# Kernel tuning notes

Hardware: AMD Instinct MI355X
Metric: run time of the kernel (lower is better)

Reference implementation:

```python
import jax, jax.numpy as jnp
import numpy as np

LAM = 0.5   # dec_init_lambda
NEG = -1e8  # attention mask fill


def gru_cell(x, h, W_ih, W_hh, b_ih, b_hh):
    # torch.nn.GRUCell math
    gi = x @ W_ih.T + b_ih
    gh = h @ W_hh.T + b_hh
    ir, iz, inn = jnp.split(gi, 3, axis=-1)
    hr, hz, hn = jnp.split(gh, 3, axis=-1)
    r = jax.nn.sigmoid(ir + hr)
    z = jax.nn.sigmoid(iz + hz)
    n = jnp.tanh(inn + r * hn)
    return (1.0 - z) * n + z * h


def setup_inputs() -> dict:
    key = jax.random.key(0)
    S, B, C, H, E, V, TY = 64, 64, 512, 512, 512, 32000, 49
    ks = jax.random.split(key, 16)
    sc = lambda d: 1.0 / float(np.sqrt(d))
    inp = {}
    inp['ctx'] = jax.random.normal(ks[0], (S, B, C), jnp.float32)
    inp['ctx_mask'] = jnp.ones((S, B), jnp.float32)
    inp['txt_ctx'] = jax.random.normal(ks[1], (B, C), jnp.float32)
    inp['y'] = jax.random.randint(ks[2], (TY, B), 0, V)
    emb = jax.random.normal(ks[3], (V, E), jnp.float32) * 0.01
    inp['emb_table'] = emb.at[0].set(0.0)  # padding_idx=0
    inp['W_ctx2ctx'] = jax.random.normal(ks[4], (C, C), jnp.float32) * sc(C)
    inp['W_hid2ctx'] = jax.random.normal(ks[5], (C, H), jnp.float32) * sc(H)
    inp['w_mlp'] = jax.random.normal(ks[6], (C,), jnp.float32) * sc(C)
    inp['W_ctx2hid'] = jax.random.normal(ks[7], (H, C), jnp.float32) * sc(C)
    inp['W_dec_init'] = jax.random.normal(ks[8], (H, C), jnp.float32) * sc(C)
    inp['W_ih0'] = jax.random.normal(ks[9], (3 * H, E), jnp.float32) * sc(E)
    inp['W_hh0'] = jax.random.normal(ks[10], (3 * H, H), jnp.float32) * sc(H)
    inp['b_ih0'] = jnp.zeros((3 * H,), jnp.float32)
    inp['b_hh0'] = jnp.zeros((3 * H,), jnp.float32)
    inp['W_ih1'] = jax.random.normal(ks[11], (3 * H, H), jnp.float32) * sc(H)
    inp['W_hh1'] = jax.random.normal(ks[12], (3 * H, H), jnp.float32) * sc(H)
    inp['b_ih1'] = jnp.zeros((3 * H,), jnp.float32)
    inp['b_hh1'] = jnp.zeros((3 * H,), jnp.float32)
    inp['W_hid2out'] = jax.random.normal(ks[13], (E, H), jnp.float32) * sc(H)
    inp['b_hid2out'] = jnp.zeros((E,), jnp.float32)  # bias_zero=True
    inp['W_out2prob'] = jax.random.normal(ks[14], (V, E), jnp.float32) * sc(E)
    inp['b_out2prob'] = jnp.zeros((V,), jnp.float32)
    return inp


def reference(ctx, ctx_mask, txt_ctx, y, emb_table,
              W_ctx2ctx, W_hid2ctx, w_mlp, W_ctx2hid, W_dec_init,
              W_ih0, W_hh0, b_ih0, b_hh0,
              W_ih1, W_hh1, b_ih1, b_hh1,
              W_hid2out, b_hid2out, W_out2prob, b_out2prob):
    # f_init: mix mean visual ctx with sentence ctx, project to h0
    mean_ctx = ctx.sum(0) / ctx_mask.sum(0)[:, None]          # (B, C)
    mixed = LAM * mean_ctx + (1.0 - LAM) * txt_ctx            # (B, C)
    h0 = jnp.tanh(mixed @ W_dec_init.T)                       # (B, H)

    # precompute ctx projection of MLP attention (ctx2ctx), shared across steps
    ctx_proj = jnp.einsum('sbc,mc->sbm', ctx, W_ctx2ctx)      # (S, B, C)

    x_seq = emb_table[y[:-1]]                                 # (T, B, E) teacher-forced inputs
    tgt = y[1:]                                               # (T, B) targets

    def step(h, xs):
        x, t = xs
        h1 = gru_cell(x, h, W_ih0, W_hh0, b_ih0, b_hh0)       # (B, H)
        q = h1 @ W_hid2ctx.T                                  # (B, C)
        scores = jnp.einsum('sbm,m->sb', jnp.tanh(ctx_proj + q[None]), w_mlp)
        scores = jnp.where(ctx_mask > 0, scores, NEG)
        alpha = jax.nn.softmax(scores, axis=0)                # (S, B) over source
        z_t = jnp.einsum('sb,sbc->bc', alpha, ctx) @ W_ctx2hid.T  # (B, H)
        h2 = gru_cell(z_t, h1, W_ih1, W_hh1, b_ih1, b_hh1)    # (B, H)
        logit = jnp.tanh(h2 @ W_hid2out.T + b_hid2out)        # (B, E)
        log_p = jax.nn.log_softmax(logit @ W_out2prob.T + b_out2prob, axis=-1)
        lp = jnp.take_along_axis(log_p, t[:, None], axis=1)[:, 0]
        loss_t = -jnp.where(t != 0, lp, 0.0).sum()            # NLLLoss(sum, ignore_index=0)
        return h2, loss_t

    _, losses = jax.lax.scan(step, h0, (x_seq, tgt))
    return losses.sum()
```

## Files before the change

kernel.cpp:

```cpp
#include <hip/hip_runtime.h>
#include <stdint.h>


using bf16x8 = __attribute__((ext_vector_type(8))) short;
using f32x4  = __attribute__((ext_vector_type(4))) float;
using s16x4  = __attribute__((ext_vector_type(4))) short;
typedef unsigned long long u64;
typedef unsigned int u32;

#define DI __device__ __forceinline__

DI short f2bf(float x){
  union { float f; uint32_t u; } v; v.f = x;
  uint32_t r = (v.u + 0x7FFFu + ((v.u >> 16) & 1u)) >> 16;
  return (short)r;
}
DI float bf2f(short s){
  union { uint32_t u; float f; } v; v.u = ((uint32_t)(unsigned short)s) << 16; return v.f;
}
DI float sigm(float x){ return __fdividef(1.f, 1.f + __expf(-x)); }
DI float ftanh(float x){ return 1.f - __fdividef(2.f, __expf(2.f*x) + 1.f); }
DI float wsum(float v){
  #pragma unroll
  for (int m = 32; m > 0; m >>= 1) v += __shfl_xor(v, m, 64);
  return v;
}
DI f32x4 mfma16(bf16x8 a, bf16x8 b, f32x4 c){
  return __builtin_amdgcn_mfma_f32_16x16x32_bf16(a, b, c, 0, 0, 0);
}

DI u32  ald32(const u32* p){ return __hip_atomic_load(p, __ATOMIC_RELAXED, __HIP_MEMORY_SCOPE_AGENT); }
DI void ast32(u32* p, u32 v){ __hip_atomic_store(p, v, __ATOMIC_RELAXED, __HIP_MEMORY_SCOPE_AGENT); }
DI u64  ald64(const u64* p){ return __hip_atomic_load(p, __ATOMIC_RELAXED, __HIP_MEMORY_SCOPE_AGENT); }
DI void ast64(u64* p, u64 v){ __hip_atomic_store(p, v, __ATOMIC_RELAXED, __HIP_MEMORY_SCOPE_AGENT); }
DI float aldf(const float* p){ return __hip_atomic_load(p, __ATOMIC_RELAXED, __HIP_MEMORY_SCOPE_AGENT); }
DI void astf(float* p, float v){ __hip_atomic_store(p, v, __ATOMIC_RELAXED, __HIP_MEMORY_SCOPE_AGENT); }

DI bf16x8 ldb(const short* __restrict__ W, int n0, int k0, int lane){
  return *(const bf16x8*)(W + (size_t)(n0 + (lane & 15)) * 512 + k0 + ((lane >> 4) << 3));
}

#define SLOT 64

DI void sig(u32* arr, int slot, u32 tok){
  if (threadIdx.x == 0){
    __builtin_amdgcn_s_waitcnt(0);
    ast32(arr + slot * SLOT, tok);
  }
}
DI void waitslots(const u32* arr, int base, int cnt, u32 tok){
  if (threadIdx.x < 64){
    for (;;){
      u32 v = (threadIdx.x < cnt) ? ald32(arr + (base + threadIdx.x) * SLOT) : tok;
      if (__all((int)(v - tok) >= 0)) break;
      __builtin_amdgcn_s_sleep(1);
    }
  }
  __syncthreads();
}


struct CvtJobs { const float* src[8]; short* dst[8]; int cum4[9]; };

__global__ __launch_bounds__(256) void k_cvt_multi(CvtJobs jb, int total4){
  int i = blockIdx.x * 256 + threadIdx.x;
  if (i >= total4) return;
  int j = 0;
  #pragma unroll
  for (int k = 0; k < 8; ++k) if (i >= jb.cum4[k + 1]) j = k + 1;
  int off = i - jb.cum4[j];
  float4 v = ((const float4*)jb.src[j])[off];
  s16x4 o; o[0] = f2bf(v.x); o[1] = f2bf(v.y); o[2] = f2bf(v.z); o[3] = f2bf(v.w);
  ((s16x4*)jb.dst[j])[off] = o;
}

__global__ __launch_bounds__(256) void k_tc(const float* __restrict__ W, short* __restrict__ WT){
  int i = blockIdx.x * 256 + threadIdx.x;
  int c = i >> 9, h = i & 511;
  WT[i] = f2bf(W[h * 512 + c]);
}

__global__ __launch_bounds__(256) void k_zero(float* __restrict__ p, int n){
  int i = blockIdx.x * 256 + threadIdx.x;
  if (i < n) p[i] = 0.f;
}

__global__ __launch_bounds__(256) void k_meanmix(const float* __restrict__ ctx, const float* __restrict__ mask,
                                                 const float* __restrict__ txt, float* __restrict__ mixed){
  int i = blockIdx.x * 256 + threadIdx.x;
  int b = i >> 9, c = i & 511;
  float s = 0.f;
  for (int t = 0; t < 64; ++t) s += ctx[(size_t)(t * 64 + b) * 512 + c];
  float dn = 0.f;
  for (int t = 0; t < 64; ++t) dn += mask[t * 64 + b];
  mixed[i] = 0.5f * (s / dn) + 0.5f * txt[i];
}

__global__ __launch_bounds__(256) void k_pack_h0(const float* __restrict__ h0, u32* __restrict__ hbf){
  int i = blockIdx.x * 256 + threadIdx.x;
  u32 lo = (u32)(unsigned short)f2bf(h0[2 * i]);
  u32 hi = (u32)(unsigned short)f2bf(h0[2 * i + 1]);
  hbf[i] = lo | (hi << 16);
}


DI bf16x8 load_a32(const float* __restrict__ A, int ld, int m0, int k0, int lane){
  const float* p = A + (size_t)(m0 + (lane & 15)) * ld + k0 + ((lane >> 4) << 3);
  bf16x8 f;
  #pragma unroll
  for (int j = 0; j < 8; ++j) f[j] = f2bf(p[j]);
  return f;
}

__global__ __launch_bounds__(256) void k_gemm_bt(const float* __restrict__ A, const short* __restrict__ W,
                                                 float* __restrict__ C, int N, int act){
  int wg = blockIdx.x * 4 + (threadIdx.x >> 6);
  int lane = threadIdx.x & 63;
  int ntiles = N >> 4;
  int mt = wg / ntiles, nt = wg - mt * ntiles;
  int m0 = mt << 4, n0 = nt << 4;
  f32x4 acc = {0.f, 0.f, 0.f, 0.f};
  for (int k = 0; k < 512; k += 32)
    acc = mfma16(load_a32(A, 512, m0, k, lane), ldb(W, n0, k, lane), acc);
  int col = n0 + (lane & 15);
  int r0 = m0 + ((lane >> 4) << 2);
  #pragma unroll
  for (int r = 0; r < 4; ++r){
    float v = acc[r];
    if (act) v = ftanh(v);
    C[(size_t)(r0 + r) * N + col] = v;
  }
}

__global__ __launch_bounds__(256) void k_gemm_bt_obf(const float* __restrict__ A, const short* __restrict__ W,
                                                     short* __restrict__ C, int N){
  int wg = blockIdx.x * 4 + (threadIdx.x >> 6);
  int lane = threadIdx.x & 63;
  int ntiles = N >> 4;
  int mt = wg / ntiles, nt = wg - mt * ntiles;
  int m0 = mt << 4, n0 = nt << 4;
  f32x4 acc = {0.f, 0.f, 0.f, 0.f};
  for (int k = 0; k < 512; k += 32)
    acc = mfma16(load_a32(A, 512, m0, k, lane), ldb(W, n0, k, lane), acc);
  int col = n0 + (lane & 15);
  int r0 = m0 + ((lane >> 4) << 2);
  #pragma unroll
  for (int r = 0; r < 4; ++r)
    C[(size_t)(r0 + r) * N + col] = f2bf(acc[r]);
}

__global__ __launch_bounds__(256) void k_gi0(const int* __restrict__ y, const float* __restrict__ emb,
                                             const short* __restrict__ W, const float* __restrict__ bias,
                                             float* __restrict__ C){
  int wg = blockIdx.x * 4 + (threadIdx.x >> 6);
  int lane = threadIdx.x & 63;
  int mt = wg / 96, nt = wg - mt * 96;
  int m0 = mt << 4, n0 = nt << 4;
  int yr = y[m0 + (lane & 15)];
  const float* arow = emb + (size_t)yr * 512;
  f32x4 acc = {0.f, 0.f, 0.f, 0.f};
  for (int k = 0; k < 512; k += 32){
    const float* p = arow + k + ((lane >> 4) << 3);
    bf16x8 a;
    #pragma unroll
    for (int j = 0; j < 8; ++j) a[j] = f2bf(p[j]);
    acc = mfma16(a, ldb(W, n0, k, lane), acc);
  }
  int col = n0 + (lane & 15);
  int r0 = m0 + ((lane >> 4) << 2);
  #pragma unroll
  for (int r = 0; r < 4; ++r)
    C[(size_t)(r0 + r) * 1536 + col] = acc[r] + bias[col];
}


struct RB {
  const float* gi0;
  const short* Whh0; const float* bhh0;
  const short* Whid2ctx;
  const short* Whh1; const float* bhh1;
  const short* Wcomb; const float* bih1;
  const short* ctx_proj;
  const float* ctx;
  const float* mask;
  const float* wmlp;
  unsigned short* h_bf;
  unsigned short* h1_bf;
  unsigned short* catt_bf;
  float* qpart;
  float* h2;
  u32* barA; u32* barC; u32* barD;
};

__global__ __launch_bounds__(256, 1) void k_recur(RB a){
  __shared__ char smem[16 * 520 * 2 + 16 * 64 * 4];
  unsigned short* sH = (unsigned short*)smem;
  float* sOut = (float*)(smem + 16 * 520 * 2);
  float* pl   = (float*)smem;
  __shared__ float qs[512];
  __shared__ float al[64];
  const int wg = blockIdx.x, tid = threadIdx.x;
  const int wv = tid >> 6, lane = tid & 63;

  auto burst16 = [&](const unsigned short* src, int row0){
    #pragma unroll
    for (int i = 0; i < 8; ++i){
      int idx = tid + i * 256;
      int r = idx >> 7, c4 = idx & 127;
      u64 v = ald64((const u64*)(src + (size_t)(row0 + r) * 512) + c4);
      *(u64*)(sH + r * 520 + c4 * 4) = v;
    }
    __syncthreads();
  };
  auto afrag = [&](int k0) -> bf16x8 {
    return *(const bf16x8*)(sH + (lane & 15) * 520 + k0 + ((lane >> 4) << 3));
  };
  auto packstore = [&](unsigned short* dst, int mrow0, int jbase){
    int r = tid >> 4, ch = tid & 15;
    float4 v = *(const float4*)&sOut[r * 64 + ch * 4];
    u64 pk = (u64)(unsigned short)f2bf(v.x)
           | ((u64)(unsigned short)f2bf(v.y) << 16)
           | ((u64)(unsigned short)f2bf(v.z) << 32)
           | ((u64)(unsigned short)f2bf(v.w) << 48);
    ast64((u64*)(dst + (size_t)(mrow0 + r) * 512 + jbase + ch * 4), pk);
  };
  auto attention = [&](int b, float maskv, const float (&w8)[8]){
    float q0 = 0.f, q1 = 0.f;
    #pragma unroll
    for (int cgi = 0; cgi < 8; ++cgi){
      u64 v = ald64((const u64*)(a.qpart + (size_t)(cgi * 64 + b) * 512) + tid);
      union { u64 u; float f[2]; } cv; cv.u = v;
      q0 += cv.f[0]; q1 += cv.f[1];
    }
    qs[2 * tid] = q0; qs[2 * tid + 1] = q1;
    __syncthreads();
    float q8[8];
    #pragma unroll
    for (int j = 0; j < 8; ++j) q8[j] = qs[lane * 8 + j];
    for (int i = 0; i < 16; ++i){
      int s = (wv << 4) + i;
      bf16x8 c8 = *(const bf16x8*)(a.ctx_proj + (size_t)((s << 6) + b) * 512 + lane * 8);
      float p = 0.f;
      #pragma unroll
      for (int j = 0; j < 8; ++j)
        p += ftanh(bf2f(c8[j]) + q8[j]) * w8[j];
      pl[s * 65 + lane] = p;
    }
    __syncthreads();
    if (tid < 64){
      const float* row = pl + tid * 65;
      float v0 = 0.f, v1 = 0.f, v2 = 0.f, v3 = 0.f;
      #pragma unroll
      for (int j = 0; j < 64; j += 4){
        v0 += row[j]; v1 += row[j + 1]; v2 += row[j + 2]; v3 += row[j + 3];
      }
      float v = (v0 + v1) + (v2 + v3);
      v = (maskv > 0.f) ? v : -100000000.0f;
      float mx = v;
      #pragma unroll
      for (int m = 32; m > 0; m >>= 1) mx = fmaxf(mx, __shfl_xor(mx, m, 64));
      float e = __expf(v - mx);
      float se = e;
      #pragma unroll
      for (int m = 32; m > 0; m >>= 1) se += __shfl_xor(se, m, 64);
      al[tid] = e / se;
    }
    __syncthreads();
    float s0 = 0.f, s1 = 0.f;
    int c0 = tid * 2;
    for (int s = 0; s < 64; ++s){
      float2 cv = *(const float2*)(a.ctx + (size_t)((s << 6) + b) * 512 + c0);
      s0 += al[s] * cv.x; s1 += al[s] * cv.y;
    }
    u32 pk = (u32)(unsigned short)f2bf(s0) | ((u32)(unsigned short)f2bf(s1) << 16);
    ast32((u32*)a.catt_bf + (size_t)b * 256 + tid, pk);
  };

  if (wg < 32){
    const int rg = wg >> 3, cg = wg & 7;
    const int mrow0 = rg << 4, jbase = cg << 6;
    const int j0 = jbase + (wv << 4);
    const int col = j0 + (lane & 15), lcol = col - jbase;
    const int lr0 = (lane >> 4) << 2;
    const int batt = wg;
    const int abase = (batt >> 4) << 3;
    const float bh0r = a.bhh0[col], bh0z = a.bhh0[512 + col], bh0n = a.bhh0[1024 + col];
    float w8[8];
    #pragma unroll
    for (int j = 0; j < 8; ++j) w8[j] = a.wmlp[lane * 8 + j];
    const float maskv = (tid < 64) ? a.mask[(tid << 6) + batt] : 0.f;
    float g0[4], g1[4], g2[4];
    {
      const float* gi = a.gi0;
      #pragma unroll
      for (int r = 0; r < 4; ++r){
        const float* gib = gi + (size_t)(mrow0 + lr0 + r) * 1536;
        g0[r] = gib[col]; g1[r] = gib[512 + col]; g2[r] = gib[1024 + col];
      }
    }
    #pragma unroll 1
    for (int t = 0; t < 48; ++t){
      const u32 tok = t + 1;
      waitslots(a.barD, rg << 3, 8, (u32)t);
      burst16(a.h_bf, mrow0);
      f32x4 aR = {0,0,0,0}, aZ = {0,0,0,0}, aN = {0,0,0,0};
      for (int k0 = 0; k0 < 512; k0 += 32){
        bf16x8 af = afrag(k0);
        aR = mfma16(af, ldb(a.Whh0, j0,        k0, lane), aR);
        aZ = mfma16(af, ldb(a.Whh0, 512 + j0,  k0, lane), aZ);
        aN = mfma16(af, ldb(a.Whh0, 1024 + j0, k0, lane), aN);
      }
      #pragma unroll
      for (int r = 0; r < 4; ++r){
        int lr = lr0 + r;
        float rr = sigm(g0[r] + aR[r] + bh0r);
        float zz = sigm(g1[r] + aZ[r] + bh0z);
        float nn = ftanh(g2[r] + rr * (aN[r] + bh0n));
        float hp = bf2f((short)sH[lr * 520 + col]);
        sOut[lr * 64 + lcol] = (1.f - zz) * nn + zz * hp;
      }
      __syncthreads();
      packstore(a.h1_bf, mrow0, jbase);
      bf16x8 qa0, qa1;
      #pragma unroll
      for (int j = 0; j < 8; ++j){
        qa0[j] = f2bf(sOut[(lane & 15) * 64 +      ((lane >> 4) << 3) + j]);
        qa1[j] = f2bf(sOut[(lane & 15) * 64 + 32 + ((lane >> 4) << 3) + j]);
      }
      #pragma unroll
      for (int nt = 0; nt < 8; ++nt){
        int n0 = (wv << 7) + (nt << 4);
        f32x4 qacc = {0,0,0,0};
        qacc = mfma16(qa0, ldb(a.Whid2ctx, n0, jbase,      lane), qacc);
        qacc = mfma16(qa1, ldb(a.Whid2ctx, n0, jbase + 32, lane), qacc);
        int qcol = n0 + (lane & 15);
        #pragma unroll
        for (int r = 0; r < 4; ++r)
          astf(a.qpart + (size_t)(cg * 64 + mrow0 + lr0 + r) * 512 + qcol, qacc[r]);
      }
      __syncthreads();
      sig(a.barA, wg, tok);
      waitslots(a.barA, abase, 8, tok);
      attention(batt, maskv, w8);
      __syncthreads();
      sig(a.barC, batt, tok);
      if (t < 47){
        const float* gi = a.gi0 + (size_t)(t + 1) * 98304;
        #pragma unroll
        for (int r = 0; r < 4; ++r){
          const float* gib = gi + (size_t)(mrow0 + lr0 + r) * 1536;
          g0[r] = gib[col]; g1[r] = gib[512 + col]; g2[r] = gib[1024 + col];
        }
      }
    }
  } else if (wg < 64){
    const int g = wg - 32;
    const int rg = g >> 3, cg = g & 7;
    const int mrow0 = rg << 4, jbase = cg << 6;
    const int j0 = jbase + (wv << 4);
    const int col = j0 + (lane & 15), lcol = col - jbase;
    const int lr0 = (lane >> 4) << 2;
    const float bcR = a.bih1[col]        + a.bhh1[col];
    const float bcZ = a.bih1[512 + col]  + a.bhh1[512 + col];
    const float biN = a.bih1[1024 + col];
    const float bhN = a.bhh1[1024 + col];
    #pragma unroll 1
    for (int t = 0; t < 48; ++t){
      const u32 tok = t + 1;
      waitslots(a.barA, rg << 3, 8, tok);
      burst16(a.h1_bf, mrow0);
      f32x4 hR = {0,0,0,0}, hZ = {0,0,0,0}, hN = {0,0,0,0};
      for (int k0 = 0; k0 < 512; k0 += 32){
        bf16x8 af = afrag(k0);
        hR = mfma16(af, ldb(a.Whh1, j0,        k0, lane), hR);
        hZ = mfma16(af, ldb(a.Whh1, 512 + j0,  k0, lane), hZ);
        hN = mfma16(af, ldb(a.Whh1, 1024 + j0, k0, lane), hN);
      }
      float hp4[4];
      #pragma unroll
      for (int r = 0; r < 4; ++r) hp4[r] = bf2f((short)sH[(lr0 + r) * 520 + col]);
      waitslots(a.barC, mrow0, 16, tok);
      burst16(a.catt_bf, mrow0);
      f32x4 iR = {0,0,0,0}, iZ = {0,0,0,0}, iN = {0,0,0,0};
      for (int k0 = 0; k0 < 512; k0 += 32){
        bf16x8 af = afrag(k0);
        iR = mfma16(af, ldb(a.Wcomb, j0,        k0, lane), iR);
        iZ = mfma16(af, ldb(a.Wcomb, 512 + j0,  k0, lane), iZ);
        iN = mfma16(af, ldb(a.Wcomb, 1024 + j0, k0, lane), iN);
      }
      float* h2t = a.h2 + (size_t)t * 32768;
      #pragma unroll
      for (int r = 0; r < 4; ++r){
        int lr = lr0 + r, b = mrow0 + lr;
        float rr = sigm(iR[r] + hR[r] + bcR);
        float zz = sigm(iZ[r] + hZ[r] + bcZ);
        float nn = ftanh(iN[r] + biN + rr * (hN[r] + bhN));
        float hv = (1.f - zz) * nn + zz * hp4[r];
        h2t[(size_t)b * 512 + col] = hv;
        sOut[lr * 64 + lcol] = hv;
      }
      __syncthreads();
      packstore(a.h_bf, mrow0, jbase);
      __syncthreads();
      sig(a.barD, g, tok);
    }
  } else {
    const int b = wg - 32;
    const int abase = (b >> 4) << 3;
    float w8[8];
    #pragma unroll
    for (int j = 0; j < 8; ++j) w8[j] = a.wmlp[lane * 8 + j];
    const float maskv = (tid < 64) ? a.mask[(tid << 6) + b] : 0.f;
    #pragma unroll 1
    for (int t = 0; t < 48; ++t){
      const u32 tok = t + 1;
      waitslots(a.barA, abase, 8, tok);
      attention(b, maskv, w8);
      __syncthreads();
      sig(a.barC, b, tok);
    }
  }
}


__global__ __launch_bounds__(256) void k_logit(const float* __restrict__ A, const short* __restrict__ W,
                                               const float* __restrict__ bias, short* __restrict__ tlb,
                                               float* __restrict__ tlf){
  int wg = blockIdx.x * 4 + (threadIdx.x >> 6);
  int lane = threadIdx.x & 63;
  int mt = wg >> 5, nt = wg & 31;
  int m0 = mt << 4, n0 = nt << 4;
  f32x4 acc = {0.f, 0.f, 0.f, 0.f};
  for (int k = 0; k < 512; k += 32)
    acc = mfma16(load_a32(A, 512, m0, k, lane), ldb(W, n0, k, lane), acc);
  int col = n0 + (lane & 15);
  int r0 = m0 + ((lane >> 4) << 2);
  #pragma unroll
  for (int r = 0; r < 4; ++r){
    float v = ftanh(acc[r] + bias[col]);
    size_t o = (size_t)(r0 + r) * 512 + col;
    tlf[o] = v; tlb[o] = f2bf(v);
  }
}

__global__ __launch_bounds__(256) void k_sumexp(const short* __restrict__ A, const short* __restrict__ B,
                                                const float* __restrict__ bias, float* __restrict__ sumexp){
  __shared__ short lA[128 * 40];
  __shared__ short lB[128 * 40];
  int bid = blockIdx.x;
  int swz = (bid & 7) * 750 + (bid >> 3);
  int bm = swz % 24, bn = swz / 24;
  int m0 = bm * 128, n0 = bn * 128;
  int tid = threadIdx.x, w = tid >> 6, lane = tid & 63;
  int mq = (w >> 1) * 64, nq = (w & 1) * 64;
  f32x4 acc[4][4];
  #pragma unroll
  for (int i = 0; i < 4; ++i)
    #pragma unroll
    for (int j = 0; j < 4; ++j) acc[i][j] = (f32x4){0.f, 0.f, 0.f, 0.f};

  for (int k0 = 0; k0 < 512; k0 += 32){
    __syncthreads();
    #pragma unroll
    for (int i = 0; i < 2; ++i){
      int idx = tid * 8 + i * 2048;
      int row = idx >> 5, colh = idx & 31;
      *(bf16x8*)&lA[row * 40 + colh] = *(const bf16x8*)(A + (size_t)(m0 + row) * 512 + k0 + colh);
      *(bf16x8*)&lB[row * 40 + colh] = *(const bf16x8*)(B + (size_t)(n0 + row) * 512 + k0 + colh);
    }
    __syncthreads();
    bf16x8 af[4], bfr[4];
    #pragma unroll
    for (int x = 0; x < 4; ++x){
      af[x]  = *(const bf16x8*)&lA[(mq + x * 16 + (lane & 15)) * 40 + ((lane >> 4) << 3)];
      bfr[x] = *(const bf16x8*)&lB[(nq + x * 16 + (lane & 15)) * 40 + ((lane >> 4) << 3)];
    }
    #pragma unroll
    for (int mi = 0; mi < 4; ++mi)
      #pragma unroll
      for (int ni = 0; ni < 4; ++ni)
        acc[mi][ni] = mfma16(af[mi], bfr[ni], acc[mi][ni]);
  }

  #pragma unroll
  for (int mi = 0; mi < 4; ++mi){
    #pragma unroll
    for (int r = 0; r < 4; ++r){
      float e = 0.f;
      #pragma unroll
      for (int ni = 0; ni < 4; ++ni){
        int col = n0 + nq + ni * 16 + (lane & 15);
        e += __expf(acc[mi][ni][r] + bias[col]);
      }
      e += __shfl_xor(e, 1, 64); e += __shfl_xor(e, 2, 64);
      e += __shfl_xor(e, 4, 64); e += __shfl_xor(e, 8, 64);
      if ((lane & 15) == 0){
        int row = m0 + mq + mi * 16 + ((lane >> 4) << 2) + r;
        atomicAdd(&sumexp[row], e);
      }
    }
  }
}

__global__ __launch_bounds__(256) void k_loss(const float* __restrict__ tlf, const float* __restrict__ Wop,
                                              const float* __restrict__ bop, const int* __restrict__ y,
                                              const float* __restrict__ sumexp, float* __restrict__ loss){
  int step = blockIdx.x;
  int w = threadIdx.x >> 6, lane = threadIdx.x & 63;
  __shared__ float accw[4];
  float part = 0.f;
  for (int b = w; b < 64; b += 4){
    int row = step * 64 + b;
    int t = y[(step + 1) * 64 + b];
    if (t != 0){
      const float* a = tlf + (size_t)row * 512 + lane * 8;
      const float* wr = Wop + (size_t)t * 512 + lane * 8;
      float d = 0.f;
      #pragma unroll
      for (int j = 0; j < 8; ++j) d += a[j] * wr[j];
      d = wsum(d);
      if (lane == 0) part += d + bop[t] - __logf(sumexp[row]);
    }
  }
  if (lane == 0) accw[w] = part;
  __syncthreads();
  if (threadIdx.x == 0) atomicAdd(loss, -(accw[0] + accw[1] + accw[2] + accw[3]));
}

__global__ void k_final(const float* __restrict__ loss, float* __restrict__ out){
  if (threadIdx.x == 0 && blockIdx.x == 0) out[0] = loss[0];
}


extern "C" void kernel_launch(void* const* d_in, const int* in_sizes, int n_in,
                              void* d_out, int out_size, void* d_ws, size_t ws_size,
                              hipStream_t stream) {
  const float* ctx       = (const float*)d_in[0];
  const float* ctx_mask  = (const float*)d_in[1];
  const float* txt_ctx   = (const float*)d_in[2];
  const int*   y         = (const int*)d_in[3];
  const float* emb       = (const float*)d_in[4];
  const float* W_ctx2ctx = (const float*)d_in[5];
  const float* W_hid2ctx = (const float*)d_in[6];
  const float* w_mlp     = (const float*)d_in[7];
  const float* W_ctx2hid = (const float*)d_in[8];
  const float* W_dec_init= (const float*)d_in[9];
  const float* W_ih0     = (const float*)d_in[10];
  const float* W_hh0     = (const float*)d_in[11];
  const float* b_ih0     = (const float*)d_in[12];
  const float* b_hh0     = (const float*)d_in[13];
  const float* W_ih1     = (const float*)d_in[14];
  const float* W_hh1     = (const float*)d_in[15];
  const float* b_ih1     = (const float*)d_in[16];
  const float* b_hh1     = (const float*)d_in[17];
  const float* W_hid2out = (const float*)d_in[18];
  const float* b_hid2out = (const float*)d_in[19];
  const float* W_out2prob= (const float*)d_in[20];
  const float* b_out2prob= (const float*)d_in[21];
  float* out = (float*)d_out;

  char* p = (char*)d_ws;
  auto alloc = [&](size_t n){ char* r = p; p += (n + 255) & ~(size_t)255; return r; };
  short* Wb_hh0     = (short*)alloc((size_t)1536 * 512 * 2);
  short* Wb_hid2ctx = (short*)alloc((size_t)512 * 512 * 2);
  short* Wb_hh1     = (short*)alloc((size_t)1536 * 512 * 2);
  short* Wb_hid2out = (short*)alloc((size_t)512 * 512 * 2);
  short* Wb_dec     = (short*)alloc((size_t)512 * 512 * 2);
  short* Wb_c2c     = (short*)alloc((size_t)512 * 512 * 2);
  short* Wb_ih0     = (short*)alloc((size_t)1536 * 512 * 2);
  short* Wb_o2p     = (short*)alloc((size_t)32000 * 512 * 2);
  short* WctT       = (short*)alloc((size_t)512 * 512 * 2);
  short* Wb_comb    = (short*)alloc((size_t)1536 * 512 * 2);
  short* ctx_projbf = (short*)alloc((size_t)4096 * 512 * 2);
  float* gi0_all    = (float*)alloc((size_t)3072 * 1536 * 4);
  float* mixed      = (float*)alloc((size_t)64 * 512 * 4);
  float* h0buf      = (float*)alloc((size_t)64 * 512 * 4);
  unsigned short* h_bf    = (unsigned short*)alloc((size_t)64 * 512 * 2);
  unsigned short* h1_bf   = (unsigned short*)alloc((size_t)64 * 512 * 2);
  unsigned short* catt_bf = (unsigned short*)alloc((size_t)64 * 512 * 2);
  float* qpart      = (float*)alloc((size_t)8 * 64 * 512 * 4);
  float* h2_all     = (float*)alloc((size_t)3072 * 512 * 4);
  short* tl_bf      = (short*)alloc((size_t)3072 * 512 * 2);
  float* tl_f       = (float*)alloc((size_t)3072 * 512 * 4);
  int nbar = 3 * 64 * SLOT;
  float* zreg       = (float*)alloc((size_t)(3073 + nbar) * 4);
  float* sumexp     = zreg;
  float* lossbuf    = zreg + 3072;
  u32* barA         = (u32*)(zreg + 3073);
  u32* barC         = barA + 64 * SLOT;
  u32* barD         = barC + 64 * SLOT;

  dim3 blk(256);
  CvtJobs jb;
  const float* srcs[8] = {W_hh0, W_hid2ctx, W_hh1, W_hid2out, W_dec_init, W_ctx2ctx, W_ih0, W_out2prob};
  short* dsts[8] = {Wb_hh0, Wb_hid2ctx, Wb_hh1, Wb_hid2out, Wb_dec, Wb_c2c, Wb_ih0, Wb_o2p};
  int sizes4[8] = {1536*512/4, 512*512/4, 1536*512/4, 512*512/4, 512*512/4, 512*512/4, 1536*512/4, 32000*512/4};
  int cum = 0;
  for (int i = 0; i < 8; ++i){ jb.src[i] = srcs[i]; jb.dst[i] = dsts[i]; jb.cum4[i] = cum; cum += sizes4[i]; }
  jb.cum4[8] = cum;
  k_cvt_multi<<<dim3((cum + 255) / 256), blk, 0, stream>>>(jb, cum);
  k_tc<<<dim3(1024), blk, 0, stream>>>(W_ctx2hid, WctT);
  k_gemm_bt_obf<<<dim3(768), blk, 0, stream>>>(W_ih1, WctT, Wb_comb, 512);
  k_meanmix<<<dim3(128), blk, 0, stream>>>(ctx, ctx_mask, txt_ctx, mixed);
  k_gemm_bt<<<dim3(32), blk, 0, stream>>>(mixed, Wb_dec, h0buf, 512, 1);
  k_pack_h0<<<dim3(64), blk, 0, stream>>>(h0buf, (u32*)h_bf);
  k_gemm_bt_obf<<<dim3(2048), blk, 0, stream>>>(ctx, Wb_c2c, ctx_projbf, 512);
  k_gi0<<<dim3(4608), blk, 0, stream>>>(y, emb, Wb_ih0, b_ih0, gi0_all);
  k_zero<<<dim3((3073 + nbar + 255) / 256), blk, 0, stream>>>(zreg, 3073 + nbar);

  RB rb;
  rb.gi0 = gi0_all;
  rb.Whh0 = Wb_hh0; rb.bhh0 = b_hh0;
  rb.Whid2ctx = Wb_hid2ctx;
  rb.Whh1 = Wb_hh1; rb.bhh1 = b_hh1;
  rb.Wcomb = Wb_comb; rb.bih1 = b_ih1;
  rb.ctx_proj = ctx_projbf; rb.ctx = ctx; rb.mask = ctx_mask; rb.wmlp = w_mlp;
  rb.h_bf = h_bf; rb.h1_bf = h1_bf; rb.catt_bf = catt_bf;
  rb.qpart = qpart; rb.h2 = h2_all;
  rb.barA = barA; rb.barC = barC; rb.barD = barD;
  void* kargs[] = { &rb };
  hipLaunchCooperativeKernel((const void*)k_recur, dim3(96), blk, kargs, 0, stream);

  k_logit<<<dim3(1536), blk, 0, stream>>>(h2_all, Wb_hid2out, b_hid2out, tl_bf, tl_f);
  k_sumexp<<<dim3(6000), blk, 0, stream>>>(tl_bf, Wb_o2p, b_out2prob, sumexp);
  k_loss<<<dim3(48), blk, 0, stream>>>(tl_f, W_out2prob, b_out2prob, y, sumexp, lossbuf);
  k_final<<<dim3(1), blk, 0, stream>>>(lossbuf, out);
}
```

Measured before the change: 2.552 ms.

## Fuse output projection and vocab sum-exp into persistent recurrence kernel

The hid2out projection and the vocabulary logsumexp GEMM now run inside the persistent recurrent kernel, on 128 extra workgroups that consume each timestep's h2 as it is produced, signalled through a new barrier array. The W_out2prob bf16 conversion also moves into those workgroups, so it overlaps with the serial recurrence instead of running as separate kernels afterward. The goal is to hide the large vocab GEMM behind the latency-bound recurrence. In exchange, the kernel launches 224 blocks with a plain launch instead of a cooperative one, relying on all blocks being co-resident for the spin-waits. It also adds zeroing kernels and per-timestep GEMMs with less reuse than the tiled LDS version.

```diff
diff --git a/kernel.cpp b/kernel.cpp
--- a/kernel.cpp
+++ b/kernel.cpp
@@ -39,6 +39,12 @@
 DI bf16x8 ldb(const short* __restrict__ W, int n0, int k0, int lane){
   return *(const bf16x8*)(W + (size_t)(n0 + (lane & 15)) * 512 + k0 + ((lane >> 4) << 3));
 }
+DI bf16x8 ldb_ald(const unsigned short* W, int n0, int k0, int lane){
+  const u64* p = (const u64*)(W + (size_t)(n0 + (lane & 15)) * 512 + k0 + ((lane >> 4) << 3));
+  union { u64 u[2]; bf16x8 f; } cv;
+  cv.u[0] = ald64(p); cv.u[1] = ald64(p + 1);
+  return cv.f;
+}
 
 #define SLOT 64
 
@@ -48,12 +54,13 @@
     ast32(arr + slot * SLOT, tok);
   }
 }
+template<int SLP>
 DI void waitslots(const u32* arr, int base, int cnt, u32 tok){
   if (threadIdx.x < 64){
     for (;;){
       u32 v = (threadIdx.x < cnt) ? ald32(arr + (base + threadIdx.x) * SLOT) : tok;
       if (__all((int)(v - tok) >= 0)) break;
-      __builtin_amdgcn_s_sleep(1);
+      __builtin_amdgcn_s_sleep(SLP);
     }
   }
   __syncthreads();
@@ -188,8 +195,15 @@
   unsigned short* h1_bf;
   unsigned short* catt_bf;
   float* qpart;
-  float* h2;
-  u32* barA; u32* barC; u32* barD;
+  unsigned short* h2bf;
+  const short* Whid2out; const float* bh2o;
+  const float* o2p_src;
+  short* o2p_bf;
+  const float* bop;
+  unsigned short* tl_bf;
+  float* tl_f;
+  float* sumexp;
+  u32* barA; u32* barC; u32* barD; u32* barE;
 };
 
 __global__ __launch_bounds__(256, 1) void k_recur(RB a){
@@ -301,7 +315,7 @@
     #pragma unroll 1
     for (int t = 0; t < 48; ++t){
       const u32 tok = t + 1;
-      waitslots(a.barD, rg << 3, 8, (u32)t);
+      waitslots<1>(a.barD, rg << 3, 8, (u32)t);
       burst16(a.h_bf, mrow0);
       f32x4 aR = {0,0,0,0}, aZ = {0,0,0,0}, aN = {0,0,0,0};
       for (int k0 = 0; k0 < 512; k0 += 32){
@@ -340,7 +354,7 @@
       }
       __syncthreads();
       sig(a.barA, wg, tok);
-      waitslots(a.barA, abase, 8, tok);
+      waitslots<1>(a.barA, abase, 8, tok);
       attention(batt, maskv, w8);
       __syncthreads();
       sig(a.barC, batt, tok);
@@ -367,7 +381,7 @@
     #pragma unroll 1
     for (int t = 0; t < 48; ++t){
       const u32 tok = t + 1;
-      waitslots(a.barA, rg << 3, 8, tok);
+      waitslots<1>(a.barA, rg << 3, 8, tok);
       burst16(a.h1_bf, mrow0);
       f32x4 hR = {0,0,0,0}, hZ = {0,0,0,0}, hN = {0,0,0,0};
       for (int k0 = 0; k0 < 512; k0 += 32){
@@ -379,7 +393,7 @@
       float hp4[4];
       #pragma unroll
       for (int r = 0; r < 4; ++r) hp4[r] = bf2f((short)sH[(lr0 + r) * 520 + col]);
-      waitslots(a.barC, mrow0, 16, tok);
+      waitslots<1>(a.barC, mrow0, 16, tok);
       burst16(a.catt_bf, mrow0);
       f32x4 iR = {0,0,0,0}, iZ = {0,0,0,0}, iN = {0,0,0,0};
       for (int k0 = 0; k0 < 512; k0 += 32){
@@ -388,23 +402,21 @@
         iZ = mfma16(af, ldb(a.Wcomb, 512 + j0,  k0, lane), iZ);
         iN = mfma16(af, ldb(a.Wcomb, 1024 + j0, k0, lane), iN);
       }
-      float* h2t = a.h2 + (size_t)t * 32768;
       #pragma unroll
       for (int r = 0; r < 4; ++r){
-        int lr = lr0 + r, b = mrow0 + lr;
+        int lr = lr0 + r;
         float rr = sigm(iR[r] + hR[r] + bcR);
         float zz = sigm(iZ[r] + hZ[r] + bcZ);
         float nn = ftanh(iN[r] + biN + rr * (hN[r] + bhN));
-        float hv = (1.f - zz) * nn + zz * hp4[r];
-        h2t[(size_t)b * 512 + col] = hv;
-        sOut[lr * 64 + lcol] = hv;
+        sOut[lr * 64 + lcol] = (1.f - zz) * nn + zz * hp4[r];
       }
       __syncthreads();
       packstore(a.h_bf, mrow0, jbase);
+      packstore(a.h2bf + (size_t)t * 32768, mrow0, jbase);
       __syncthreads();
       sig(a.barD, g, tok);
     }
-  } else {
+  } else if (wg < 96){
     const int b = wg - 32;
     const int abase = (b >> 4) << 3;
     float w8[8];
@@ -414,93 +426,98 @@
     #pragma unroll 1
     for (int t = 0; t < 48; ++t){
       const u32 tok = t + 1;
-      waitslots(a.barA, abase, 8, tok);
+      waitslots<1>(a.barA, abase, 8, tok);
       attention(b, maskv, w8);
       __syncthreads();
       sig(a.barC, b, tok);
     }
+  } else if (wg < 128){
+    const int vl = wg - 96;
+    const int rg = vl >> 3, cg = vl & 7;
+    const int mrow0 = rg << 4, jbase = cg << 6;
+    const int j0 = jbase + (wv << 4);
+    const int col = j0 + (lane & 15), lcol = col - jbase;
+    const int lr0 = (lane >> 4) << 2;
+    const float bo = a.bh2o[col];
+    #pragma unroll 1
+    for (int t = 0; t < 48; ++t){
+      const u32 tok = t + 1;
+      waitslots<16>(a.barD, rg << 3, 8, tok);
+      const unsigned short* h2t = a.h2bf + (size_t)t * 32768;
+      f32x4 acc = {0,0,0,0};
+      for (int k0 = 0; k0 < 512; k0 += 32)
+        acc = mfma16(ldb_ald(h2t, mrow0, k0, lane), ldb(a.Whid2out, j0, k0, lane), acc);
+      #pragma unroll
+      for (int r = 0; r < 4; ++r){
+        float v = ftanh(acc[r] + bo);
+        int row = (t << 6) + mrow0 + lr0 + r;
+        a.tl_f[(size_t)row * 512 + col] = v;
+        sOut[(lr0 + r) * 64 + lcol] = v;
+      }
+      __syncthreads();
+      packstore(a.tl_bf + (size_t)t * 32768, mrow0, jbase);
+      __syncthreads();
+      sig(a.barE, vl, tok);
+    }
+  } else {
+    const int vg = wg - 128;
+    for (int c = vg; c < 125; c += 96){
+      const float* src = a.o2p_src + (size_t)c * 256 * 512;
+      short* dst = a.o2p_bf + (size_t)c * 256 * 512;
+      for (int i = tid; i < 32768; i += 256){
+        float4 v = ((const float4*)src)[i];
+        s16x4 o; o[0] = f2bf(v.x); o[1] = f2bf(v.y); o[2] = f2bf(v.z); o[3] = f2bf(v.w);
+        ((s16x4*)dst)[i] = o;
+      }
+    }
+    __syncthreads();
+    #pragma unroll 1
+    for (int t = 0; t < 48; ++t){
+      const u32 tok = t + 1;
+      waitslots<16>(a.barE, 0, 32, tok);
+      const unsigned short* tlt = a.tl_bf + (size_t)t * 32768;
+      #pragma unroll 1
+      for (int c = vg; c < 125; c += 96){
+        const int nwave = c * 256 + wv * 64;
+        float bos[4];
+        #pragma unroll
+        for (int ni = 0; ni < 4; ++ni) bos[ni] = a.bop[nwave + ni * 16 + (lane & 15)];
+        f32x4 acc[4][4];
+        #pragma unroll
+        for (int i = 0; i < 4; ++i)
+          #pragma unroll
+          for (int j = 0; j < 4; ++j) acc[i][j] = (f32x4){0.f, 0.f, 0.f, 0.f};
+        for (int k0 = 0; k0 < 512; k0 += 32){
+          bf16x8 af[4], bw[4];
+          #pragma unroll
+          for (int mi = 0; mi < 4; ++mi) af[mi] = ldb_ald(tlt, mi << 4, k0, lane);
+          #pragma unroll
+          for (int ni = 0; ni < 4; ++ni) bw[ni] = ldb(a.o2p_bf, nwave + (ni << 4), k0, lane);
+          #pragma unroll
+          for (int mi = 0; mi < 4; ++mi)
+            #pragma unroll
+            for (int ni = 0; ni < 4; ++ni)
+              acc[mi][ni] = mfma16(af[mi], bw[ni], acc[mi][ni]);
+        }
+        #pragma unroll
+        for (int mi = 0; mi < 4; ++mi){
+          #pragma unroll
+          for (int r = 0; r < 4; ++r){
+            float e = 0.f;
+            #pragma unroll
+            for (int ni = 0; ni < 4; ++ni)
+              e += __expf(acc[mi][ni][r] + bos[ni]);
+            e += __shfl_xor(e, 1, 64); e += __shfl_xor(e, 2, 64);
+            e += __shfl_xor(e, 4, 64); e += __shfl_xor(e, 8, 64);
+            if ((lane & 15) == 0)
+              atomicAdd(&a.sumexp[(t << 6) + (mi << 4) + ((lane >> 4) << 2) + r], e);
+          }
+        }
+      }
+    }
   }
 }
 
-
-__global__ __launch_bounds__(256) void k_logit(const float* __restrict__ A, const short* __restrict__ W,
-                                               const float* __restrict__ bias, short* __restrict__ tlb,
-                                               float* __restrict__ tlf){
-  int wg = blockIdx.x * 4 + (threadIdx.x >> 6);
-  int lane = threadIdx.x & 63;
-  int mt = wg >> 5, nt = wg & 31;
-  int m0 = mt << 4, n0 = nt << 4;
-  f32x4 acc = {0.f, 0.f, 0.f, 0.f};
-  for (int k = 0; k < 512; k += 32)
-    acc = mfma16(load_a32(A, 512, m0, k, lane), ldb(W, n0, k, lane), acc);
-  int col = n0 + (lane & 15);
-  int r0 = m0 + ((lane >> 4) << 2);
-  #pragma unroll
-  for (int r = 0; r < 4; ++r){
-    float v = ftanh(acc[r] + bias[col]);
-    size_t o = (size_t)(r0 + r) * 512 + col;
-    tlf[o] = v; tlb[o] = f2bf(v);
-  }
-}
-
-__global__ __launch_bounds__(256) void k_sumexp(const short* __restrict__ A, const short* __restrict__ B,
-                                                const float* __restrict__ bias, float* __restrict__ sumexp){
-  __shared__ short lA[128 * 40];
-  __shared__ short lB[128 * 40];
-  int bid = blockIdx.x;
-  int swz = (bid & 7) * 750 + (bid >> 3);
-  int bm = swz % 24, bn = swz / 24;
-  int m0 = bm * 128, n0 = bn * 128;
-  int tid = threadIdx.x, w = tid >> 6, lane = tid & 63;
-  int mq = (w >> 1) * 64, nq = (w & 1) * 64;
-  f32x4 acc[4][4];
-  #pragma unroll
-  for (int i = 0; i < 4; ++i)
-    #pragma unroll
-    for (int j = 0; j < 4; ++j) acc[i][j] = (f32x4){0.f, 0.f, 0.f, 0.f};
-
-  for (int k0 = 0; k0 < 512; k0 += 32){
-    __syncthreads();
-    #pragma unroll
-    for (int i = 0; i < 2; ++i){
-      int idx = tid * 8 + i * 2048;
-      int row = idx >> 5, colh = idx & 31;
-      *(bf16x8*)&lA[row * 40 + colh] = *(const bf16x8*)(A + (size_t)(m0 + row) * 512 + k0 + colh);
-      *(bf16x8*)&lB[row * 40 + colh] = *(const bf16x8*)(B + (size_t)(n0 + row) * 512 + k0 + colh);
-    }
-    __syncthreads();
-    bf16x8 af[4], bfr[4];
-    #pragma unroll
-    for (int x = 0; x < 4; ++x){
-      af[x]  = *(const bf16x8*)&lA[(mq + x * 16 + (lane & 15)) * 40 + ((lane >> 4) << 3)];
-      bfr[x] = *(const bf16x8*)&lB[(nq + x * 16 + (lane & 15)) * 40 + ((lane >> 4) << 3)];
-    }
-    #pragma unroll
-    for (int mi = 0; mi < 4; ++mi)
-      #pragma unroll
-      for (int ni = 0; ni < 4; ++ni)
-        acc[mi][ni] = mfma16(af[mi], bfr[ni], acc[mi][ni]);
-  }
-
-  #pragma unroll
-  for (int mi = 0; mi < 4; ++mi){
-    #pragma unroll
-    for (int r = 0; r < 4; ++r){
-      float e = 0.f;
-      #pragma unroll
-      for (int ni = 0; ni < 4; ++ni){
-        int col = n0 + nq + ni * 16 + (lane & 15);
-        e += __expf(acc[mi][ni][r] + bias[col]);
-      }
-      e += __shfl_xor(e, 1, 64); e += __shfl_xor(e, 2, 64);
-      e += __shfl_xor(e, 4, 64); e += __shfl_xor(e, 8, 64);
-      if ((lane & 15) == 0){
-        int row = m0 + mq + mi * 16 + ((lane >> 4) << 2) + r;
-        atomicAdd(&sumexp[row], e);
-      }
-    }
-  }
-}
 
 __global__ __launch_bounds__(256) void k_loss(const float* __restrict__ tlf, const float* __restrict__ Wop,
                                               const float* __restrict__ bop, const int* __restrict__ y,
@@ -579,22 +596,23 @@
   unsigned short* h1_bf   = (unsigned short*)alloc((size_t)64 * 512 * 2);
   unsigned short* catt_bf = (unsigned short*)alloc((size_t)64 * 512 * 2);
   float* qpart      = (float*)alloc((size_t)8 * 64 * 512 * 4);
-  float* h2_all     = (float*)alloc((size_t)3072 * 512 * 4);
-  short* tl_bf      = (short*)alloc((size_t)3072 * 512 * 2);
+  unsigned short* h2bf = (unsigned short*)alloc((size_t)3072 * 512 * 2);
+  unsigned short* tl_bf = (unsigned short*)alloc((size_t)3072 * 512 * 2);
   float* tl_f       = (float*)alloc((size_t)3072 * 512 * 4);
-  int nbar = 3 * 64 * SLOT;
+  int nbar = 4 * 64 * SLOT;
   float* zreg       = (float*)alloc((size_t)(3073 + nbar) * 4);
   float* sumexp     = zreg;
   float* lossbuf    = zreg + 3072;
   u32* barA         = (u32*)(zreg + 3073);
   u32* barC         = barA + 64 * SLOT;
   u32* barD         = barC + 64 * SLOT;
+  u32* barE         = barD + 64 * SLOT;
 
   dim3 blk(256);
   CvtJobs jb;
-  const float* srcs[8] = {W_hh0, W_hid2ctx, W_hh1, W_hid2out, W_dec_init, W_ctx2ctx, W_ih0, W_out2prob};
-  short* dsts[8] = {Wb_hh0, Wb_hid2ctx, Wb_hh1, Wb_hid2out, Wb_dec, Wb_c2c, Wb_ih0, Wb_o2p};
-  int sizes4[8] = {1536*512/4, 512*512/4, 1536*512/4, 512*512/4, 512*512/4, 512*512/4, 1536*512/4, 32000*512/4};
+  const float* srcs[8] = {W_hh0, W_hid2ctx, W_hh1, W_hid2out, W_dec_init, W_ctx2ctx, W_ih0, W_hh0};
+  short* dsts[8] = {Wb_hh0, Wb_hid2ctx, Wb_hh1, Wb_hid2out, Wb_dec, Wb_c2c, Wb_ih0, Wb_hh0};
+  int sizes4[8] = {1536*512/4, 512*512/4, 1536*512/4, 512*512/4, 512*512/4, 512*512/4, 1536*512/4, 0};
   int cum = 0;
   for (int i = 0; i < 8; ++i){ jb.src[i] = srcs[i]; jb.dst[i] = dsts[i]; jb.cum4[i] = cum; cum += sizes4[i]; }
   jb.cum4[8] = cum;
@@ -607,6 +625,9 @@
   k_gemm_bt_obf<<<dim3(2048), blk, 0, stream>>>(ctx, Wb_c2c, ctx_projbf, 512);
   k_gi0<<<dim3(4608), blk, 0, stream>>>(y, emb, Wb_ih0, b_ih0, gi0_all);
   k_zero<<<dim3((3073 + nbar + 255) / 256), blk, 0, stream>>>(zreg, 3073 + nbar);
+  k_zero<<<dim3(3072), blk, 0, stream>>>((float*)h2bf, 786432);
+  k_zero<<<dim3(3072), blk, 0, stream>>>((float*)tl_bf, 786432);
+  k_zero<<<dim3(6144), blk, 0, stream>>>(tl_f, 1572864);
 
   RB rb;
   rb.gi0 = gi0_all;
@@ -616,13 +637,13 @@
   rb.Wcomb = Wb_comb; rb.bih1 = b_ih1;
   rb.ctx_proj = ctx_projbf; rb.ctx = ctx; rb.mask = ctx_mask; rb.wmlp = w_mlp;
   rb.h_bf = h_bf; rb.h1_bf = h1_bf; rb.catt_bf = catt_bf;
-  rb.qpart = qpart; rb.h2 = h2_all;
-  rb.barA = barA; rb.barC = barC; rb.barD = barD;
-  void* kargs[] = { &rb };
-  hipLaunchCooperativeKernel((const void*)k_recur, dim3(96), blk, kargs, 0, stream);
-
-  k_logit<<<dim3(1536), blk, 0, stream>>>(h2_all, Wb_hid2out, b_hid2out, tl_bf, tl_f);
-  k_sumexp<<<dim3(6000), blk, 0, stream>>>(tl_bf, Wb_o2p, b_out2prob, sumexp);
+  rb.qpart = qpart; rb.h2bf = h2bf;
+  rb.Whid2out = Wb_hid2out; rb.bh2o = b_hid2out;
+  rb.o2p_src = W_out2prob; rb.o2p_bf = Wb_o2p; rb.bop = b_out2prob;
+  rb.tl_bf = tl_bf; rb.tl_f = tl_f; rb.sumexp = sumexp;
+  rb.barA = barA; rb.barC = barC; rb.barD = barD; rb.barE = barE;
+  k_recur<<<dim3(224), blk, 0, stream>>>(rb);
+
   k_loss<<<dim3(48), blk, 0, stream>>>(tl_f, W_out2prob, b_out2prob, y, sumexp, lossbuf);
   k_final<<<dim3(1), blk, 0, stream>>>(lossbuf, out);
 }
```

Result: slower. 4.757 ms (+86.4%).
